# Optimization experiments

Hardware: AMD Instinct MI355X
Metric: run time of the kernel (lower is better)

## Reference

```python
import jax, jax.numpy as jnp
import numpy as np

LEVEL_SIZES = [256, 128, 64, 32, 16]  # FPN map sizes for a 1024x1024 image
B, N, C = 16, 64, 8
EPS = 1e-8


def setup_inputs() -> dict:
    key = jax.random.key(0)
    ks = jax.random.split(key, 9)
    inp = {}
    for l, s in enumerate(LEVEL_SIZES):
        # attention maps must be in (0,1) for binary_cross_entropy
        inp[f"attn{l}"] = jax.random.uniform(ks[l], (B, C, s, s), jnp.float32, 1e-4, 1.0 - 1e-4)
    # boxes: x1,y1 in-image; widths/heights in [8, 512] px so all levels get boxes
    x1 = jax.random.uniform(ks[5], (B, N)) * (1024.0 - 16.0)
    y1 = jax.random.uniform(ks[6], (B, N)) * (1024.0 - 16.0)
    dw = 8.0 + jax.random.uniform(ks[7], (B, N)) * 504.0
    dh = 8.0 + jax.random.uniform(ks[8], (B, N)) * 504.0
    x2 = jnp.minimum(x1 + dw, 1024.0)
    y2 = jnp.minimum(y1 + dh, 1024.0)
    inp["bboxs"] = jnp.stack([x1, y1, x2, y2], axis=-1)  # [B, N, 4]
    inp["img_h"] = 1024
    inp["img_w"] = 1024
    inp["alpha"] = 5
    inp["beta"] = 2
    return inp


def reference(attn0, attn1, attn2, attn3, attn4, bboxs, img_h, img_w, alpha, beta):
    attns = [attn0, attn1, attn2, attn3, attn4]
    h = float(img_h)
    w = float(img_w)
    x1, y1, x2, y2 = bboxs[..., 0], bboxs[..., 1], bboxs[..., 2], bboxs[..., 3]  # each [B, N]
    # original validity filter: coords <= image bounds
    valid = (x1 <= w) & (y1 <= h) & (x2 <= w) & (y2 <= h)  # [B, N]
    area = jnp.abs((x2 - x1) * (y2 - y1))  # [B, N]

    per_level = []  # list of [B, C] losses
    for l, a in enumerate(attns):
        _, _, Hl, Wl = a.shape
        side = 2.0 ** (l + alpha)
        min_a = side ** 2
        max_a = (side * beta) ** 2
        sel = valid & (area >= min_a) & (area <= max_a)  # [B, N]

        sx = Wl / w
        sy = Hl / h
        # integer pixel bounds: int() truncation == floor for nonneg coords, then clamp
        xi1 = jnp.maximum(jnp.floor(x1 * sx), 0.0)
        yi1 = jnp.maximum(jnp.floor(y1 * sy), 0.0)
        xi2 = jnp.minimum(jnp.ceil(x2 * sx) + 1.0, float(Wl))
        yi2 = jnp.minimum(jnp.ceil(y2 * sy) + 1.0, float(Hl))

        ys = jnp.arange(Hl, dtype=jnp.float32)
        xs = jnp.arange(Wl, dtype=jnp.float32)
        # separable per-box row/col indicators; fold the level selector into rows
        row = ((ys[None, None, :] >= yi1[..., None]) & (ys[None, None, :] < yi2[..., None])
               & sel[..., None]).astype(jnp.float32)  # [B, N, Hl]
        col = ((xs[None, None, :] >= xi1[..., None]) & (xs[None, None, :] < xi2[..., None])
               ).astype(jnp.float32)  # [B, N, Wl]
        # OR over boxes == (sum of outer products) > 0
        mask_gt = (jnp.einsum('bnh,bnw->bhw', row, col) > 0).astype(jnp.float32)  # [B, Hl, Wl]

        t = mask_gt[:, None, :, :]  # broadcast over channels
        p = a  # [B, C, Hl, Wl]
        bce = jnp.mean(-(t * jnp.log(p) + (1.0 - t) * jnp.log(1.0 - p)), axis=(2, 3))  # [B, C]
        inter = 2.0 * jnp.sum(p * t, axis=(2, 3)) + EPS
        union = jnp.sum(p, axis=(2, 3)) + jnp.sum(t, axis=(2, 3)) + EPS
        dice = 1.0 - inter / union  # [B, C]
        per_level.append(0.5 * bce + 0.5 * dice)

    losses = jnp.stack(per_level, axis=1)  # [B, L, C]
    per_image = losses.mean(axis=(1, 2))  # [B]
    has_box = valid.any(axis=1)
    per_image = jnp.where(has_box, per_image, 0.0)
    return per_image.mean(keepdims=True)  # shape [1]
```

## Files before the change

### kernel.cpp

```cpp
#include <hip/hip_runtime.h>
#include <cstdint>

#define NBOX 64
#define NB   16
#define NC   8
#define EPSF 1e-8f
#define LN2F 0.69314718055994531f


__device__ __forceinline__ unsigned long long range_mask(int a, int e, int base) {
    int lo = a - base; lo = lo < 0 ? 0 : (lo > 64 ? 64 : lo);
    int hi = e - base; hi = hi < 0 ? 0 : (hi > 64 ? 64 : hi);
    if (hi <= lo) return 0ULL;
    unsigned long long hm = (hi >= 64) ? ~0ULL : ((1ULL << hi) - 1ULL);
    unsigned long long lm = (1ULL << lo) - 1ULL;
    return hm & ~lm;
}

struct SharedBuf {
    int rx1[NBOX], rx2[NBOX], ry1[NBOX], ry2[NBOX];
    unsigned long long rowm[64][4];
    float red[4][4];
};

template<int LVL>
__device__ __forceinline__ void scan_level(
    SharedBuf& sh, int rel,
    const float* __restrict__ attn, const float* __restrict__ bboxs,
    float w, float h, int alpha, int beta, float* __restrict__ acc)
{
    constexpr int Hl   = 256 >> LVL;
    constexpr int P    = Hl * Hl;
    constexpr int TPX  = (P < 4096) ? P : 4096;
    constexpr int NT   = P / TPX;
    constexpr int NROWS = TPX / Hl;
    constexpr int LOGW = 8 - LVL;
    constexpr int W64  = (Hl >= 64) ? (Hl / 64) : 1;
    constexpr int NBATCH = (TPX + 1023) / 1024;

    const int tile = (NT == 1) ? 0 : (rel % NT);
    const int bc   = (NT == 1) ? rel : (rel / NT);
    const int c = bc & 7, b = bc >> 3;
    const int tid = threadIdx.x;

    const float side  = (float)(1 << (LVL + alpha));
    const float min_a = side * side;
    const float sbb   = side * (float)beta;
    const float max_a = sbb * sbb;
    const float sx = (float)Hl / w;
    const float sy = (float)Hl / h;

    if (tid < NBOX) {
        const float* bb = bboxs + (size_t)(b * NBOX + tid) * 4;
        float x1 = bb[0], y1 = bb[1], x2 = bb[2], y2 = bb[3];
        bool valid = (x1 <= w) && (y1 <= h) && (x2 <= w) && (y2 <= h);
        float area = fabsf((x2 - x1) * (y2 - y1));
        bool sel = valid && (area >= min_a) && (area <= max_a);
        sh.rx1[tid] = (int)fmaxf(floorf(x1 * sx), 0.f);
        sh.rx2[tid] = (int)fminf(ceilf(x2 * sx) + 1.f, (float)Hl);
        int yi1 = (int)fmaxf(floorf(y1 * sy), 0.f);
        int yi2 = (int)fminf(ceilf(y2 * sy) + 1.f, (float)Hl);
        sh.ry1[tid] = sel ? yi1 : 0;
        sh.ry2[tid] = sel ? yi2 : 0;
    }
    __syncthreads();

    const int start = tile * TPX;
    const int r0    = tile * NROWS;
    float my_t = 0.f;
    if (tid < NROWS) {
        const int hh = r0 + tid;
        unsigned long long m0 = 0, m1 = 0, m2 = 0, m3 = 0;
        for (int n = 0; n < NBOX; ++n) {
            if (hh >= sh.ry1[n] && hh < sh.ry2[n]) {
                int a = sh.rx1[n], e = sh.rx2[n];
                m0 |= range_mask(a, e, 0);
                if (W64 > 1) m1 |= range_mask(a, e, 64);
                if (W64 > 2) { m2 |= range_mask(a, e, 128); m3 |= range_mask(a, e, 192); }
            }
        }
        sh.rowm[tid][0] = m0; my_t += (float)__popcll(m0);
        if (W64 > 1) { sh.rowm[tid][1] = m1; my_t += (float)__popcll(m1); }
        if (W64 > 2) { sh.rowm[tid][2] = m2; my_t += (float)__popcll(m2);
                       sh.rowm[tid][3] = m3; my_t += (float)__popcll(m3); }
    }
    __syncthreads();

    const float* p = attn + (size_t)(b * NC + c) * P;
    float4 v[NBATCH];
#pragma unroll
    for (int k = 0; k < NBATCH; ++k) {
        int off = k * 1024 + tid * 4;
        if (off < TPX) v[k] = *(const float4*)(p + start + off);
    }

    float l2s[NBATCH], psA[NBATCH], ptA[NBATCH];
#pragma unroll
    for (int k = 0; k < NBATCH; ++k) { l2s[k] = 0.f; psA[k] = 0.f; ptA[k] = 0.f; }

#pragma unroll
    for (int k = 0; k < NBATCH; ++k) {
        int off = k * 1024 + tid * 4;
        if (off < TPX) {
            int i = start + off;
            int hr = (i >> LOGW) - r0;
            int ww = i & (Hl - 1);
            unsigned long long wd = sh.rowm[hr][(W64 == 1) ? 0 : (ww >> 6)];
            unsigned int bits = (unsigned int)(wd >> (ww & 63)) & 0xFu;
            float4 vv = v[k];
            { float pv = vv.x; bool t = bits & 1u; l2s[k] -= __log2f(t ? pv : 1.f - pv); psA[k] += pv; if (t) ptA[k] += pv; }
            { float pv = vv.y; bool t = bits & 2u; l2s[k] -= __log2f(t ? pv : 1.f - pv); psA[k] += pv; if (t) ptA[k] += pv; }
            { float pv = vv.z; bool t = bits & 4u; l2s[k] -= __log2f(t ? pv : 1.f - pv); psA[k] += pv; if (t) ptA[k] += pv; }
            { float pv = vv.w; bool t = bits & 8u; l2s[k] -= __log2f(t ? pv : 1.f - pv); psA[k] += pv; if (t) ptA[k] += pv; }
        }
    }

    float bce = 0.f, psum = 0.f, ptsum = 0.f;
#pragma unroll
    for (int k = 0; k < NBATCH; ++k) { bce += l2s[k]; psum += psA[k]; ptsum += ptA[k]; }
    bce *= LN2F;

    for (int off = 32; off > 0; off >>= 1) {
        bce   += __shfl_down(bce,   off, 64);
        psum  += __shfl_down(psum,  off, 64);
        ptsum += __shfl_down(ptsum, off, 64);
        my_t  += __shfl_down(my_t,  off, 64);
    }
    if ((tid & 63) == 0) {
        int wv = tid >> 6;
        sh.red[wv][0] = bce; sh.red[wv][1] = psum; sh.red[wv][2] = ptsum; sh.red[wv][3] = my_t;
    }
    __syncthreads();
    if (tid == 0) {
        float* dst = acc + ((size_t)((LVL * NB + b) * NC + c)) * 4;
        atomicAdd(dst + 0, sh.red[0][0] + sh.red[1][0] + sh.red[2][0] + sh.red[3][0]);
        atomicAdd(dst + 1, sh.red[0][1] + sh.red[1][1] + sh.red[2][1] + sh.red[3][1]);
        atomicAdd(dst + 2, sh.red[0][2] + sh.red[1][2] + sh.red[2][2] + sh.red[3][2]);
        atomicAdd(dst + 3, sh.red[0][3] + sh.red[1][3] + sh.red[2][3] + sh.red[3][3]);
    }
}

__global__ __launch_bounds__(256)
void k_scan(const float* __restrict__ a0, const float* __restrict__ a1,
            const float* __restrict__ a2, const float* __restrict__ a3,
            const float* __restrict__ a4,
            const float* __restrict__ bboxs,
            const int* __restrict__ ih_p, const int* __restrict__ iw_p,
            const int* __restrict__ alpha_p, const int* __restrict__ beta_p,
            float* __restrict__ acc) {
    __shared__ SharedBuf sh;
    const float w = (float)iw_p[0], h = (float)ih_p[0];
    const int alpha = alpha_p[0], beta = beta_p[0];
    const int bid = blockIdx.x;
    if      (bid < 2048) scan_level<0>(sh, bid,        a0, bboxs, w, h, alpha, beta, acc);
    else if (bid < 2560) scan_level<1>(sh, bid - 2048, a1, bboxs, w, h, alpha, beta, acc);
    else if (bid < 2688) scan_level<2>(sh, bid - 2560, a2, bboxs, w, h, alpha, beta, acc);
    else if (bid < 2816) scan_level<3>(sh, bid - 2688, a3, bboxs, w, h, alpha, beta, acc);
    else                 scan_level<4>(sh, bid - 2816, a4, bboxs, w, h, alpha, beta, acc);
}

__global__ void k_final(const float* __restrict__ acc,
                        const float* __restrict__ bboxs,
                        const int* __restrict__ ih_p, const int* __restrict__ iw_p,
                        float* __restrict__ out) {
    const int tid = threadIdx.x;
    __shared__ float pimg[NB];
    const float w = (float)iw_p[0], h = (float)ih_p[0];
    if (tid < NB) pimg[tid] = 0.f;
    __syncthreads();
    for (int combo = tid; combo < 640; combo += 256) {
        int l = combo >> 7;
        int bc = combo & 127;
        const float* a = acc + (size_t)combo * 4;
        int HH = 256 >> l;
        float invP = 1.f / (float)(HH * HH);
        float bce = a[0] * invP;
        float dice = 1.f - (2.f * a[2] + EPSF) / (a[1] + a[3] + EPSF);
        atomicAdd(&pimg[bc >> 3], 0.5f * bce + 0.5f * dice);
    }
    __syncthreads();
    if (tid < NB) {
        const int b = tid;
        bool has = false;
        const float* bb = bboxs + (size_t)b * NBOX * 4;
        for (int n = 0; n < NBOX; ++n) {
            float x1 = bb[n * 4 + 0], y1 = bb[n * 4 + 1];
            float x2 = bb[n * 4 + 2], y2 = bb[n * 4 + 3];
            if (x1 <= w && y1 <= h && x2 <= w && y2 <= h) { has = true; break; }
        }
        pimg[b] = has ? pimg[b] * (1.f / 40.f) : 0.f;
    }
    __syncthreads();
    if (tid == 0) {
        float t = 0.f;
        for (int i = 0; i < NB; ++i) t += pimg[i];
        out[0] = t * (1.f / (float)NB);
    }
}

extern "C" void kernel_launch(void* const* d_in, const int* in_sizes, int n_in,
                              void* d_out, int out_size, void* d_ws, size_t ws_size,
                              hipStream_t stream) {
    const float* a0 = (const float*)d_in[0];
    const float* a1 = (const float*)d_in[1];
    const float* a2 = (const float*)d_in[2];
    const float* a3 = (const float*)d_in[3];
    const float* a4 = (const float*)d_in[4];
    const float* bboxs = (const float*)d_in[5];
    const int* ih = (const int*)d_in[6];
    const int* iw = (const int*)d_in[7];
    const int* al = (const int*)d_in[8];
    const int* be = (const int*)d_in[9];

    float* acc = (float*)d_ws;

    hipMemsetAsync(acc, 0, 2560 * sizeof(float), stream);
    k_scan<<<2944, 256, 0, stream>>>(a0, a1, a2, a3, a4, bboxs, ih, iw, al, be, acc);
    k_final<<<1, 256, 0, stream>>>(acc, bboxs, ih, iw, (float*)d_out);
}
```

Before: 118.2 us.

## Hoist attn loads before mask build, parallelize row masks, write per-block partials

The attention tile loads are issued at the start of each block, so memory latency overlaps the box setup and row-mask construction. Row-mask building is now split across four wavefronts, each scanning 16 boxes and merging its result with shared-memory atomicOr, where before only one wavefront scanned all 64 boxes. Global float atomics and the memset launch are dropped: each block writes a float4 partial, and the final kernel sums the tiles for each (level, b, c). This costs an extra sync plus shared atomics, and more partial reads in the final kernel.

```diff
diff --git a/kernel.cpp b/kernel.cpp
--- a/kernel.cpp
+++ b/kernel.cpp
@@ -19,93 +19,101 @@
 
 struct SharedBuf {
     int rx1[NBOX], rx2[NBOX], ry1[NBOX], ry2[NBOX];
-    unsigned long long rowm[64][4];
+    unsigned long long rowm[64];
     float red[4][4];
 };
 
 template<int LVL>
 __device__ __forceinline__ void scan_level(
-    SharedBuf& sh, int rel,
+    SharedBuf& sh, int rel, int bid,
     const float* __restrict__ attn, const float* __restrict__ bboxs,
-    float w, float h, int alpha, int beta, float* __restrict__ acc)
+    float w, float h, int alpha, int beta, float4* __restrict__ partials)
 {
-    constexpr int Hl   = 256 >> LVL;
-    constexpr int P    = Hl * Hl;
-    constexpr int TPX  = (P < 4096) ? P : 4096;
-    constexpr int NT   = P / TPX;
+    constexpr int Hl    = 256 >> LVL;
+    constexpr int P     = Hl * Hl;
+    constexpr int TPX   = (P < 4096) ? P : 4096;
+    constexpr int NT    = P / TPX;
     constexpr int NROWS = TPX / Hl;
-    constexpr int LOGW = 8 - LVL;
-    constexpr int W64  = (Hl >= 64) ? (Hl / 64) : 1;
+    constexpr int LOGW  = 8 - LVL;
+    constexpr int W64   = (Hl >= 64) ? (Hl / 64) : 1;
     constexpr int NBATCH = (TPX + 1023) / 1024;
 
     const int tile = (NT == 1) ? 0 : (rel % NT);
     const int bc   = (NT == 1) ? rel : (rel / NT);
     const int c = bc & 7, b = bc >> 3;
     const int tid = threadIdx.x;
-
-    const float side  = (float)(1 << (LVL + alpha));
-    const float min_a = side * side;
-    const float sbb   = side * (float)beta;
-    const float max_a = sbb * sbb;
-    const float sx = (float)Hl / w;
-    const float sy = (float)Hl / h;
-
+    const int start = tile * TPX;
+    const int r0    = tile * NROWS;
+
+    const float* p = attn + (size_t)(b * NC + c) * P + start;
+    float4 v[NBATCH];
+#pragma unroll
+    for (int k = 0; k < NBATCH; ++k) {
+        int off = k * 1024 + tid * 4;
+        if (off < TPX) v[k] = *(const float4*)(p + off);
+    }
+
+    if (tid < NROWS * W64) sh.rowm[tid] = 0ULL;
     if (tid < NBOX) {
-        const float* bb = bboxs + (size_t)(b * NBOX + tid) * 4;
-        float x1 = bb[0], y1 = bb[1], x2 = bb[2], y2 = bb[3];
-        bool valid = (x1 <= w) && (y1 <= h) && (x2 <= w) && (y2 <= h);
-        float area = fabsf((x2 - x1) * (y2 - y1));
+        const float side  = (float)(1 << (LVL + alpha));
+        const float min_a = side * side;
+        const float sbb   = side * (float)beta;
+        const float max_a = sbb * sbb;
+        const float sx = (float)Hl / w;
+        const float sy = (float)Hl / h;
+        float4 bb = *(const float4*)(bboxs + (size_t)(b * NBOX + tid) * 4);
+        bool valid = (bb.x <= w) && (bb.y <= h) && (bb.z <= w) && (bb.w <= h);
+        float area = fabsf((bb.z - bb.x) * (bb.w - bb.y));
         bool sel = valid && (area >= min_a) && (area <= max_a);
-        sh.rx1[tid] = (int)fmaxf(floorf(x1 * sx), 0.f);
-        sh.rx2[tid] = (int)fminf(ceilf(x2 * sx) + 1.f, (float)Hl);
-        int yi1 = (int)fmaxf(floorf(y1 * sy), 0.f);
-        int yi2 = (int)fminf(ceilf(y2 * sy) + 1.f, (float)Hl);
+        sh.rx1[tid] = (int)fmaxf(floorf(bb.x * sx), 0.f);
+        sh.rx2[tid] = (int)fminf(ceilf(bb.z * sx) + 1.f, (float)Hl);
+        int yi1 = (int)fmaxf(floorf(bb.y * sy), 0.f);
+        int yi2 = (int)fminf(ceilf(bb.w * sy) + 1.f, (float)Hl);
         sh.ry1[tid] = sel ? yi1 : 0;
         sh.ry2[tid] = sel ? yi2 : 0;
     }
     __syncthreads();
 
-    const int start = tile * TPX;
-    const int r0    = tile * NROWS;
+    {
+        const int g = tid >> 6;
+        const int r = tid & 63;
+        if (r < NROWS) {
+            const int hh = r0 + r;
+            unsigned long long m[W64];
+#pragma unroll
+            for (int wi = 0; wi < W64; ++wi) m[wi] = 0ULL;
+            const int n0 = g * 16;
+            for (int n = n0; n < n0 + 16; ++n) {
+                if (hh >= sh.ry1[n] && hh < sh.ry2[n]) {
+                    int a = sh.rx1[n], e = sh.rx2[n];
+#pragma unroll
+                    for (int wi = 0; wi < W64; ++wi) m[wi] |= range_mask(a, e, wi * 64);
+                }
+            }
+#pragma unroll
+            for (int wi = 0; wi < W64; ++wi)
+                if (m[wi]) atomicOr(&sh.rowm[r * W64 + wi], m[wi]);
+        }
+    }
+    __syncthreads();
+
     float my_t = 0.f;
     if (tid < NROWS) {
-        const int hh = r0 + tid;
-        unsigned long long m0 = 0, m1 = 0, m2 = 0, m3 = 0;
-        for (int n = 0; n < NBOX; ++n) {
-            if (hh >= sh.ry1[n] && hh < sh.ry2[n]) {
-                int a = sh.rx1[n], e = sh.rx2[n];
-                m0 |= range_mask(a, e, 0);
-                if (W64 > 1) m1 |= range_mask(a, e, 64);
-                if (W64 > 2) { m2 |= range_mask(a, e, 128); m3 |= range_mask(a, e, 192); }
-            }
-        }
-        sh.rowm[tid][0] = m0; my_t += (float)__popcll(m0);
-        if (W64 > 1) { sh.rowm[tid][1] = m1; my_t += (float)__popcll(m1); }
-        if (W64 > 2) { sh.rowm[tid][2] = m2; my_t += (float)__popcll(m2);
-                       sh.rowm[tid][3] = m3; my_t += (float)__popcll(m3); }
-    }
-    __syncthreads();
-
-    const float* p = attn + (size_t)(b * NC + c) * P;
-    float4 v[NBATCH];
-#pragma unroll
-    for (int k = 0; k < NBATCH; ++k) {
-        int off = k * 1024 + tid * 4;
-        if (off < TPX) v[k] = *(const float4*)(p + start + off);
+#pragma unroll
+        for (int wi = 0; wi < W64; ++wi)
+            my_t += (float)__popcll(sh.rowm[tid * W64 + wi]);
     }
 
     float l2s[NBATCH], psA[NBATCH], ptA[NBATCH];
 #pragma unroll
     for (int k = 0; k < NBATCH; ++k) { l2s[k] = 0.f; psA[k] = 0.f; ptA[k] = 0.f; }
-
 #pragma unroll
     for (int k = 0; k < NBATCH; ++k) {
         int off = k * 1024 + tid * 4;
         if (off < TPX) {
-            int i = start + off;
-            int hr = (i >> LOGW) - r0;
-            int ww = i & (Hl - 1);
-            unsigned long long wd = sh.rowm[hr][(W64 == 1) ? 0 : (ww >> 6)];
+            int hr = off >> LOGW;
+            int ww = off & (Hl - 1);
+            unsigned long long wd = sh.rowm[hr * W64 + ((W64 == 1) ? 0 : (ww >> 6))];
             unsigned int bits = (unsigned int)(wd >> (ww & 63)) & 0xFu;
             float4 vv = v[k];
             { float pv = vv.x; bool t = bits & 1u; l2s[k] -= __log2f(t ? pv : 1.f - pv); psA[k] += pv; if (t) ptA[k] += pv; }
@@ -114,11 +122,9 @@
             { float pv = vv.w; bool t = bits & 8u; l2s[k] -= __log2f(t ? pv : 1.f - pv); psA[k] += pv; if (t) ptA[k] += pv; }
         }
     }
-
     float bce = 0.f, psum = 0.f, ptsum = 0.f;
 #pragma unroll
     for (int k = 0; k < NBATCH; ++k) { bce += l2s[k]; psum += psA[k]; ptsum += ptA[k]; }
-    bce *= LN2F;
 
     for (int off = 32; off > 0; off >>= 1) {
         bce   += __shfl_down(bce,   off, 64);
@@ -132,11 +138,12 @@
     }
     __syncthreads();
     if (tid == 0) {
-        float* dst = acc + ((size_t)((LVL * NB + b) * NC + c)) * 4;
-        atomicAdd(dst + 0, sh.red[0][0] + sh.red[1][0] + sh.red[2][0] + sh.red[3][0]);
-        atomicAdd(dst + 1, sh.red[0][1] + sh.red[1][1] + sh.red[2][1] + sh.red[3][1]);
-        atomicAdd(dst + 2, sh.red[0][2] + sh.red[1][2] + sh.red[2][2] + sh.red[3][2]);
-        atomicAdd(dst + 3, sh.red[0][3] + sh.red[1][3] + sh.red[2][3] + sh.red[3][3]);
+        float4 o;
+        o.x = (sh.red[0][0] + sh.red[1][0] + sh.red[2][0] + sh.red[3][0]) * LN2F;
+        o.y =  sh.red[0][1] + sh.red[1][1] + sh.red[2][1] + sh.red[3][1];
+        o.z =  sh.red[0][2] + sh.red[1][2] + sh.red[2][2] + sh.red[3][2];
+        o.w =  sh.red[0][3] + sh.red[1][3] + sh.red[2][3] + sh.red[3][3];
+        partials[bid] = o;
     }
 }
 
@@ -147,19 +154,19 @@
             const float* __restrict__ bboxs,
             const int* __restrict__ ih_p, const int* __restrict__ iw_p,
             const int* __restrict__ alpha_p, const int* __restrict__ beta_p,
-            float* __restrict__ acc) {
+            float4* __restrict__ partials) {
     __shared__ SharedBuf sh;
     const float w = (float)iw_p[0], h = (float)ih_p[0];
     const int alpha = alpha_p[0], beta = beta_p[0];
     const int bid = blockIdx.x;
-    if      (bid < 2048) scan_level<0>(sh, bid,        a0, bboxs, w, h, alpha, beta, acc);
-    else if (bid < 2560) scan_level<1>(sh, bid - 2048, a1, bboxs, w, h, alpha, beta, acc);
-    else if (bid < 2688) scan_level<2>(sh, bid - 2560, a2, bboxs, w, h, alpha, beta, acc);
-    else if (bid < 2816) scan_level<3>(sh, bid - 2688, a3, bboxs, w, h, alpha, beta, acc);
-    else                 scan_level<4>(sh, bid - 2816, a4, bboxs, w, h, alpha, beta, acc);
-}
-
-__global__ void k_final(const float* __restrict__ acc,
+    if      (bid < 2048) scan_level<0>(sh, bid,        bid, a0, bboxs, w, h, alpha, beta, partials);
+    else if (bid < 2560) scan_level<1>(sh, bid - 2048, bid, a1, bboxs, w, h, alpha, beta, partials);
+    else if (bid < 2688) scan_level<2>(sh, bid - 2560, bid, a2, bboxs, w, h, alpha, beta, partials);
+    else if (bid < 2816) scan_level<3>(sh, bid - 2688, bid, a3, bboxs, w, h, alpha, beta, partials);
+    else                 scan_level<4>(sh, bid - 2816, bid, a4, bboxs, w, h, alpha, beta, partials);
+}
+
+__global__ void k_final(const float4* __restrict__ partials,
                         const float* __restrict__ bboxs,
                         const int* __restrict__ ih_p, const int* __restrict__ iw_p,
                         float* __restrict__ out) {
@@ -168,15 +175,22 @@
     const float w = (float)iw_p[0], h = (float)ih_p[0];
     if (tid < NB) pimg[tid] = 0.f;
     __syncthreads();
+    const int ntl[5]  = {16, 4, 1, 1, 1};
+    const int base[5] = {0, 2048, 2560, 2688, 2816};
     for (int combo = tid; combo < 640; combo += 256) {
-        int l = combo >> 7;
+        int l  = combo >> 7;
         int bc = combo & 127;
-        const float* a = acc + (size_t)combo * 4;
+        int cnt = ntl[l];
+        const float4* s0 = partials + base[l] + bc * cnt;
+        float sb = 0.f, sp = 0.f, st = 0.f, sc = 0.f;
+        for (int t = 0; t < cnt; ++t) {
+            float4 x = s0[t];
+            sb += x.x; sp += x.y; st += x.z; sc += x.w;
+        }
         int HH = 256 >> l;
         float invP = 1.f / (float)(HH * HH);
-        float bce = a[0] * invP;
-        float dice = 1.f - (2.f * a[2] + EPSF) / (a[1] + a[3] + EPSF);
-        atomicAdd(&pimg[bc >> 3], 0.5f * bce + 0.5f * dice);
+        float dice = 1.f - (2.f * st + EPSF) / (sp + sc + EPSF);
+        atomicAdd(&pimg[bc >> 3], 0.5f * sb * invP + 0.5f * dice);
     }
     __syncthreads();
     if (tid < NB) {
@@ -212,9 +226,8 @@
     const int* al = (const int*)d_in[8];
     const int* be = (const int*)d_in[9];
 
-    float* acc = (float*)d_ws;
-
-    hipMemsetAsync(acc, 0, 2560 * sizeof(float), stream);
-    k_scan<<<2944, 256, 0, stream>>>(a0, a1, a2, a3, a4, bboxs, ih, iw, al, be, acc);
-    k_final<<<1, 256, 0, stream>>>(acc, bboxs, ih, iw, (float*)d_out);
-}
+    float4* partials = (float4*)d_ws;
+
+    k_scan<<<2944, 256, 0, stream>>>(a0, a1, a2, a3, a4, bboxs, ih, iw, al, be, partials);
+    k_final<<<1, 256, 0, stream>>>(partials, bboxs, ih, iw, (float*)d_out);
+}
```

After: 105.5 us. -10.8%, faster.
